# Kernel optimization log

Hardware: AMD Instinct MI355X
Metric: run time of the kernel (lower is better)

Reference implementation:

```python
import jax, jax.numpy as jnp
import numpy as np

N_NODES = 20000
N_EDGES = 160000
F_IN = 128
H1 = 1024  # 128 * out_channels
H2 = 512   # 64 * out_channels
OUT = 8    # out_channels


def graph_conv(x, src, dst, w_rel, b_rel, w_root):
    # PyG GraphConv(aggr='mean'): out = lin_rel(mean_{j->i} x_j) + lin_root(x_i)
    n = x.shape[0]
    agg = jax.ops.segment_sum(x[src], dst, num_segments=n)          # [N, F_in]
    deg = jax.ops.segment_sum(jnp.ones((src.shape[0],), x.dtype), dst, num_segments=n)
    mean = agg / jnp.maximum(deg, 1.0)[:, None]
    return mean @ w_rel + b_rel + x @ w_root


def setup_inputs() -> dict:
    key = jax.random.key(0)
    ks = jax.random.split(key, 12)
    x = jax.random.normal(ks[0], (N_NODES, F_IN), dtype=jnp.float32)
    edge_index = jax.random.randint(ks[1], (2, N_EDGES), 0, N_NODES, dtype=jnp.int64)

    def lin(k, fi, fo):
        return jax.random.normal(k, (fi, fo), dtype=jnp.float32) / np.sqrt(fi)

    return {
        "x": x,
        "edge_index": edge_index,
        "w1_rel": lin(ks[2], F_IN, H1), "b1": jnp.zeros((H1,), jnp.float32), "w1_root": lin(ks[3], F_IN, H1),
        "w2_rel": lin(ks[4], H1, H2), "b2": jnp.zeros((H2,), jnp.float32), "w2_root": lin(ks[5], H1, H2),
        "wmu_rel": lin(ks[6], H2, OUT), "bmu": jnp.zeros((OUT,), jnp.float32), "wmu_root": lin(ks[7], H2, OUT),
        "wls_rel": lin(ks[8], H2, OUT), "bls": jnp.zeros((OUT,), jnp.float32), "wls_root": lin(ks[9], H2, OUT),
    }


def reference(x, edge_index, w1_rel, b1, w1_root, w2_rel, b2, w2_root,
              wmu_rel, bmu, wmu_root, wls_rel, bls, wls_root):
    src, dst = edge_index[0], edge_index[1]
    h = jax.nn.relu(graph_conv(x, src, dst, w1_rel, b1, w1_root))
    h = jax.nn.relu(graph_conv(h, src, dst, w2_rel, b2, w2_root))
    mu = graph_conv(h, src, dst, wmu_rel, bmu, wmu_root)
    logstd = graph_conv(h, src, dst, wls_rel, bls, wls_root)
    return (mu, logstd)
```

## Files before the change

### kernel.cpp

```cpp
#include <hip/hip_runtime.h>

typedef __attribute__((ext_vector_type(8))) short short8;
typedef __attribute__((ext_vector_type(4))) float f32x4;
typedef unsigned long long u64;

__device__ __forceinline__ unsigned short f2bf(float f) {
  union { float f; unsigned u; } v; v.f = f;
  unsigned u = v.u;
  unsigned r = (u + 0x7FFFu + ((u >> 16) & 1u)) >> 16;
  return (unsigned short)r;
}
__device__ __forceinline__ float bf2f(unsigned short s) {
  union { unsigned u; float f; } v; v.u = ((unsigned)s) << 16;
  return v.f;
}

__device__ __forceinline__ void gl_lds16(const unsigned short* g, unsigned short* l) {
  __builtin_amdgcn_global_load_lds(
      (const __attribute__((address_space(1))) void*)g,
      (__attribute__((address_space(3))) void*)l, 16, 0, 0);
}


__device__ __forceinline__ void ttile(const float* __restrict__ src, int Nw,
                                      unsigned short* __restrict__ dst, int ldd,
                                      int rowoff, int coloff,
                                      int tileIdx, int tilesN, float (*tile)[33]) {
  int tk = tileIdx / tilesN, tn = tileIdx % tilesN;
  int k0 = tk * 32, n0 = tn * 32;
  int tx = threadIdx.x & 31, ty = threadIdx.x >> 5;
#pragma unroll
  for (int s = 0; s < 4; ++s)
    tile[ty + s * 8][tx] = src[(size_t)(k0 + ty + s * 8) * Nw + n0 + tx];
  __syncthreads();
#pragma unroll
  for (int s = 0; s < 4; ++s)
    dst[(size_t)(rowoff + n0 + ty + s * 8) * ldd + coloff + k0 + tx] =
        f2bf(tile[tx][ty + s * 8]);
}

__global__ void prep_kernel(int* deg, int* cursor, int n, int* flag,
                            const float* __restrict__ x, unsigned short* __restrict__ xb,
                            int total4,
                            const float* __restrict__ w1_rel, const float* __restrict__ w1_root,
                            const float* __restrict__ w2_rel, const float* __restrict__ w2_root,
                            const float* __restrict__ wmu_rel, const float* __restrict__ wmu_root,
                            const float* __restrict__ wls_rel, const float* __restrict__ wls_root,
                            unsigned short* __restrict__ Bt1,
                            unsigned short* __restrict__ Bt2,
                            unsigned short* __restrict__ Bt3) {
  __shared__ float tile[32][33];
  int b = blockIdx.x;
  if (b >= 1408) {
    int b4 = (b - 1408) * 1024;
#pragma unroll
    for (int s = 0; s < 4; ++s) {
      int i4 = b4 + s * 256 + threadIdx.x;
      if (i4 < total4) {
        float4 v = reinterpret_cast<const float4*>(x)[i4];
        ushort4 o;
        o.x = f2bf(v.x); o.y = f2bf(v.y); o.z = f2bf(v.z); o.w = f2bf(v.w);
        reinterpret_cast<ushort4*>(xb)[i4] = o;
      }
    }
    return;
  }
  if (b >= 1344) {
    int i = (b - 1344) * blockDim.x + threadIdx.x;
    int stride = 64 * blockDim.x;
    for (int j = i; j < n; j += stride) { deg[j] = 0; cursor[j] = 0; }
    if (i == 0) *flag = 1;
    return;
  }
  if (b < 128)       ttile(w1_rel, 1024, Bt1, 256, 0, 0, b, 32, tile);
  else if (b < 256)  ttile(w1_root, 1024, Bt1, 256, 0, 128, b - 128, 32, tile);
  else if (b < 768)  ttile(w2_rel, 512, Bt2, 1024, 0, 0, b - 256, 16, tile);
  else if (b < 1280) ttile(w2_root, 512, Bt2, 1024, 512, 0, b - 768, 16, tile);
  else {
    int idx = (b - 1280) * 256 + threadIdx.x;
    int nn = idx >> 9, k = idx & 511;
    float v;
    if (nn < 8) v = wmu_rel[(size_t)k * 8 + nn];
    else if (nn < 16) v = wmu_root[(size_t)k * 8 + (nn - 8)];
    else if (nn < 24) v = wls_rel[(size_t)k * 8 + (nn - 16)];
    else v = wls_root[(size_t)k * 8 + (nn - 24)];
    Bt3[(size_t)nn * 512 + k] = f2bf(v);
  }
}

__global__ void detect_kernel(const long long* p, int nslots, int n_nodes, int* flag) {
  int i = blockIdx.x * blockDim.x + threadIdx.x;
  if (i < nslots) {
    long long v = p[i];
    if (v < 0 || v >= n_nodes) atomicAnd(flag, 0);
  }
}

__device__ __forceinline__ int edge_at(const void* p, int is64, size_t idx) {
  return is64 ? (int)((const long long*)p)[idx] : ((const int*)p)[idx];
}

__global__ void count_kernel(const void* edges, int E, const int* flag, int* deg) {
  int is64 = *flag;
  int i = blockIdx.x * blockDim.x + threadIdx.x;
  int stride = gridDim.x * blockDim.x;
  for (int e = i; e < E; e += stride) {
    int d = edge_at(edges, is64, (size_t)E + e);
    atomicAdd(&deg[d], 1);
  }
}

__global__ void scan_kernel(const int* __restrict__ deg, int* __restrict__ rs,
                            float* __restrict__ invdeg, int n) {
  __shared__ int ssum[1024];
  int tid = threadIdx.x;
  int chunk = (n + 1023) >> 10;
  int start = tid * chunk;
  int end = min(start + chunk, n);
  int s = 0;
  for (int i = start; i < end; ++i) s += deg[i];
  ssum[tid] = s;
  __syncthreads();
  for (int off = 1; off < 1024; off <<= 1) {
    int t = (tid >= off) ? ssum[tid - off] : 0;
    __syncthreads();
    ssum[tid] += t;
    __syncthreads();
  }
  int run = (tid ? ssum[tid - 1] : 0);
  if (tid == 0) rs[0] = 0;
  for (int i = start; i < end; ++i) {
    int d = deg[i];
    run += d;
    rs[i + 1] = run;
    invdeg[i] = 1.0f / fmaxf((float)d, 1.0f);
  }
}

__global__ void fill_kernel(const void* edges, int E, const int* flag,
                            const int* __restrict__ rs, int* cursor, int* col_src) {
  int is64 = *flag;
  int i = blockIdx.x * blockDim.x + threadIdx.x;
  int stride = gridDim.x * blockDim.x;
  for (int e = i; e < E; e += stride) {
    int d = edge_at(edges, is64, (size_t)E + e);
    int s = edge_at(edges, is64, (size_t)e);
    int p = atomicAdd(&cursor[d], 1);
    col_src[rs[d] + p] = s;
  }
}


__global__ void agg1_kernel(const unsigned short* __restrict__ xb,
                            const int* __restrict__ rs, const int* __restrict__ cs,
                            const float* __restrict__ invdeg,
                            unsigned short* __restrict__ A1, int M) {
  int node = blockIdx.x * 4 + (threadIdx.x >> 6);
  if (node >= M) return;
  int c0 = (threadIdx.x & 63) * 2;
  float a0 = 0.f, a1 = 0.f;
  int e1 = rs[node + 1];
  for (int e = rs[node]; e < e1; ++e) {
    unsigned w = *reinterpret_cast<const unsigned*>(xb + (size_t)cs[e] * 128 + c0);
    a0 += bf2f((unsigned short)(w & 0xffff));
    a1 += bf2f((unsigned short)(w >> 16));
  }
  float inv = invdeg[node];
  unsigned root = *reinterpret_cast<const unsigned*>(xb + (size_t)node * 128 + c0);
  unsigned mean = (unsigned)f2bf(a0 * inv) | ((unsigned)f2bf(a1 * inv) << 16);
  *reinterpret_cast<unsigned*>(A1 + (size_t)node * 256 + c0) = mean;
  *reinterpret_cast<unsigned*>(A1 + (size_t)node * 256 + 128 + c0) = root;
}

__global__ void agg2_kernel(const unsigned short* __restrict__ P2,
                            const int* __restrict__ rs, const int* __restrict__ cs,
                            const float* __restrict__ invdeg,
                            const float* __restrict__ b2,
                            unsigned short* __restrict__ h2, int M) {
  int node = blockIdx.x * 2 + (threadIdx.x >> 6);
  if (node >= M) return;
  int f0 = (threadIdx.x & 63) * 8;
  float acc[8];
#pragma unroll
  for (int v = 0; v < 8; ++v) acc[v] = 0.f;
  int e1 = rs[node + 1];
  for (int e = rs[node]; e < e1; ++e) {
    int s = cs[e];
    uint4 w = *reinterpret_cast<const uint4*>(P2 + (size_t)s * 1024 + f0);
    acc[0] += bf2f((unsigned short)(w.x & 0xffff));
    acc[1] += bf2f((unsigned short)(w.x >> 16));
    acc[2] += bf2f((unsigned short)(w.y & 0xffff));
    acc[3] += bf2f((unsigned short)(w.y >> 16));
    acc[4] += bf2f((unsigned short)(w.z & 0xffff));
    acc[5] += bf2f((unsigned short)(w.z >> 16));
    acc[6] += bf2f((unsigned short)(w.w & 0xffff));
    acc[7] += bf2f((unsigned short)(w.w >> 16));
  }
  float inv = invdeg[node];
  uint4 wr = *reinterpret_cast<const uint4*>(P2 + (size_t)node * 1024 + 512 + f0);
  float rt[8] = {
    bf2f((unsigned short)(wr.x & 0xffff)), bf2f((unsigned short)(wr.x >> 16)),
    bf2f((unsigned short)(wr.y & 0xffff)), bf2f((unsigned short)(wr.y >> 16)),
    bf2f((unsigned short)(wr.z & 0xffff)), bf2f((unsigned short)(wr.z >> 16)),
    bf2f((unsigned short)(wr.w & 0xffff)), bf2f((unsigned short)(wr.w >> 16))};
  unsigned short o[8];
#pragma unroll
  for (int v = 0; v < 8; ++v)
    o[v] = f2bf(fmaxf(acc[v] * inv + rt[v] + b2[f0 + v], 0.f));
  uint4 pk;
  pk.x = (unsigned)o[0] | ((unsigned)o[1] << 16);
  pk.y = (unsigned)o[2] | ((unsigned)o[3] << 16);
  pk.z = (unsigned)o[4] | ((unsigned)o[5] << 16);
  pk.w = (unsigned)o[6] | ((unsigned)o[7] << 16);
  *reinterpret_cast<uint4*>(h2 + (size_t)node * 512 + f0) = pk;
}

__global__ void head_agg_kernel(const float* __restrict__ P3,
                                const int* __restrict__ rs, const int* __restrict__ cs,
                                const float* __restrict__ invdeg,
                                const float* __restrict__ bmu, const float* __restrict__ bls,
                                float* __restrict__ outmu, float* __restrict__ outls, int M) {
  int idx = blockIdx.x * blockDim.x + threadIdx.x;
  int node = idx >> 4;
  int c = idx & 15;
  if (node >= M) return;
  int relc = (c < 8) ? c : (16 + (c - 8));
  float acc = 0.f;
  int e1 = rs[node + 1];
  for (int e = rs[node]; e < e1; ++e) acc += P3[(size_t)cs[e] * 32 + relc];
  float v = acc * invdeg[node] + P3[(size_t)node * 32 + relc + 8]
          + ((c < 8) ? bmu[c] : bls[c - 8]);
  if (c < 8) outmu[(size_t)node * 8 + c] = v;
  else outls[(size_t)node * 8 + (c - 8)] = v;
}

__launch_bounds__(256, 4)
__global__ void gemm_db_kernel(const unsigned short* __restrict__ A, int lda,
                               const unsigned short* __restrict__ Bt, int ldb,
                               const float* __restrict__ bias,
                               void* __restrict__ outp, int ldo,
                               int M, int N, int K, int relu, int out_f32, int gx) {
  __shared__ unsigned short As[2 * 4096];
  __shared__ unsigned short Bs[2 * 4096];
  const int tid = threadIdx.x;
  const int lane = tid & 63;
  const int w = tid >> 6;
  const int wr = w >> 1, wc = w & 1;
  const int lr = lane & 15, lk = lane >> 4;
  const int sw8 = (lk ^ ((lr >> 1) & 3)) * 8;

  int nwg = gridDim.x, orig = blockIdx.x;
  int q = nwg >> 3, r = nwg & 7;
  int xcd = orig & 7, lid = orig >> 3;
  int swz = (xcd < r ? xcd * (q + 1) : r * (q + 1) + (xcd - r) * q) + lid;
  int m0 = (swz / gx) * 128, n0 = (swz % gx) * 128;

  f32x4 acc[4][4];
#pragma unroll
  for (int i = 0; i < 4; ++i)
#pragma unroll
    for (int j = 0; j < 4; ++j) acc[i][j] = (f32x4)0.0f;

  const int r0 = tid >> 2;
  const int slog = ((tid & 3) ^ ((r0 >> 1) & 3)) * 8;
  const unsigned short* gA = A + (size_t)(m0 + r0) * lda + slog;
  const unsigned short* gB = Bt + (size_t)(n0 + r0) * ldb + slog;
  const size_t a64 = (size_t)64 * lda, b64 = (size_t)64 * ldb;
  unsigned short* wa = As + w * 512;
  unsigned short* wb = Bs + w * 512;

  auto STG = [&](int s, int t) {
    const unsigned short* a = gA + (size_t)t * 32;
    const unsigned short* b = gB + (size_t)t * 32;
    gl_lds16(a, wa + s * 4096);
    gl_lds16(a + a64, wa + s * 4096 + 2048);
    gl_lds16(b, wb + s * 4096);
    gl_lds16(b + b64, wb + s * 4096 + 2048);
  };

  const int nt = K >> 5;
  STG(0, 0);
  __syncthreads();

  int buf = 0;
  for (int t = 0; t < nt; ++t) {
    if (t + 1 < nt) STG(buf ^ 1, t + 1);
    const unsigned short* as_ = As + buf * 4096;
    const unsigned short* bs_ = Bs + buf * 4096;
    short8 af[4], bf[4];
#pragma unroll
    for (int i = 0; i < 4; ++i) {
      af[i] = *reinterpret_cast<const short8*>(&as_[(wr * 64 + i * 16 + lr) * 32 + sw8]);
      bf[i] = *reinterpret_cast<const short8*>(&bs_[(wc * 64 + i * 16 + lr) * 32 + sw8]);
    }
    __builtin_amdgcn_s_setprio(1);
#pragma unroll
    for (int i = 0; i < 4; ++i)
#pragma unroll
      for (int j = 0; j < 4; ++j)
        acc[i][j] = __builtin_amdgcn_mfma_f32_16x16x32_bf16(af[i], bf[j], acc[i][j], 0, 0, 0);
    __builtin_amdgcn_s_setprio(0);
    if (t + 1 < nt) __syncthreads();
    buf ^= 1;
  }

#pragma unroll
  for (int i = 0; i < 4; ++i) {
    int row_b = m0 + wr * 64 + i * 16 + lk * 4;
#pragma unroll
    for (int j = 0; j < 4; ++j) {
      int col = n0 + wc * 64 + j * 16 + lr;
      float bv = bias ? bias[col] : 0.f;
#pragma unroll
      for (int rr = 0; rr < 4; ++rr) {
        int row = row_b + rr;
        if (row < M) {
          float v = acc[i][j][rr] + bv;
          if (relu) v = fmaxf(v, 0.f);
          if (out_f32) ((float*)outp)[(size_t)row * ldo + col] = v;
          else ((unsigned short*)outp)[(size_t)row * ldo + col] = f2bf(v);
        }
      }
    }
  }
}

__launch_bounds__(256, 3)
__global__ void gemm_heads_kernel(const unsigned short* __restrict__ A,
                                  const unsigned short* __restrict__ Bt3,
                                  float* __restrict__ P3, int M) {
  __shared__ unsigned short Bs[16 * 1024];
  __shared__ unsigned short As[2 * 4096];
  const int tid = threadIdx.x;
  const int lane = tid & 63;
  const int w = tid >> 6;
  const int lr = lane & 15, lk = lane >> 4;
  const int sw8 = (lk ^ ((lr >> 1) & 3)) * 8;

  int nwg = gridDim.x, orig = blockIdx.x;
  int q = nwg >> 3, r = nwg & 7;
  int xcd = orig & 7, lid = orig >> 3;
  int swz = (xcd < r ? xcd * (q + 1) : r * (q + 1) + (xcd - r) * q) + lid;
  int m0 = swz * 128;

  for (int i = 0; i < 8; ++i) {
    int j = i * 256 + tid;
    int n = j >> 6, p = j & 63;
    int x = (n >> 1) & 3;
    uint4 v = *reinterpret_cast<const uint4*>(Bt3 + (size_t)n * 512 + ((p & ~3) | ((p & 3) ^ x)) * 8);
    *reinterpret_cast<uint4*>(&Bs[(p >> 2) * 1024 + n * 32 + (p & 3) * 8]) = v;
  }

  f32x4 acc[2][2];
#pragma unroll
  for (int i = 0; i < 2; ++i)
#pragma unroll
    for (int j = 0; j < 2; ++j) acc[i][j] = (f32x4)0.0f;

  const int r0 = tid >> 2;
  const int slog = ((tid & 3) ^ ((r0 >> 1) & 3)) * 8;
  const unsigned short* gA = A + (size_t)(m0 + r0) * 512 + slog;
  const size_t a64 = (size_t)64 * 512;
  unsigned short* wa = As + w * 512;

  auto STG = [&](int s, int t) {
    const unsigned short* a = gA + (size_t)t * 32;
    gl_lds16(a, wa + s * 4096);
    gl_lds16(a + a64, wa + s * 4096 + 2048);
  };

  STG(0, 0);
  __syncthreads();

  int buf = 0;
  const int nt = 16;
  for (int t = 0; t < nt; ++t) {
    if (t + 1 < nt) STG(buf ^ 1, t + 1);
    const unsigned short* as_ = As + buf * 4096;
    short8 af[2], bf[2];
#pragma unroll
    for (int i = 0; i < 2; ++i) {
      af[i] = *reinterpret_cast<const short8*>(&as_[(w * 32 + i * 16 + lr) * 32 + sw8]);
      bf[i] = *reinterpret_cast<const short8*>(&Bs[t * 1024 + (i * 16 + lr) * 32 + sw8]);
    }
#pragma unroll
    for (int i = 0; i < 2; ++i)
#pragma unroll
      for (int j = 0; j < 2; ++j)
        acc[i][j] = __builtin_amdgcn_mfma_f32_16x16x32_bf16(af[i], bf[j], acc[i][j], 0, 0, 0);
    if (t + 1 < nt) __syncthreads();
    buf ^= 1;
  }

#pragma unroll
  for (int i = 0; i < 2; ++i) {
    int row_b = m0 + w * 32 + i * 16 + lk * 4;
#pragma unroll
    for (int j = 0; j < 2; ++j) {
      int col = j * 16 + lr;
#pragma unroll
      for (int rr = 0; rr < 4; ++rr) {
        int row = row_b + rr;
        if (row < M) P3[(size_t)row * 32 + col] = acc[i][j][rr];
      }
    }
  }
}


extern "C" void kernel_launch(void* const* d_in, const int* in_sizes, int n_in,
                              void* d_out, int out_size, void* d_ws, size_t ws_size,
                              hipStream_t stream) {
  const float* x = (const float*)d_in[0];
  const void* edge = d_in[1];
  const float* w1_rel = (const float*)d_in[2];
  const float* b1 = (const float*)d_in[3];
  const float* w1_root = (const float*)d_in[4];
  const float* w2_rel = (const float*)d_in[5];
  const float* b2 = (const float*)d_in[6];
  const float* w2_root = (const float*)d_in[7];
  const float* wmu_rel = (const float*)d_in[8];
  const float* bmu = (const float*)d_in[9];
  const float* wmu_root = (const float*)d_in[10];
  const float* wls_rel = (const float*)d_in[11];
  const float* bls = (const float*)d_in[12];
  const float* wls_root = (const float*)d_in[13];

  const int FIN = 128, H1 = 1024, H2 = 512;
  const int M = in_sizes[0] / FIN;
  const int E = in_sizes[1] / 2;
  const int Mpad = ((M + 127) / 128) * 128;
  const int gy = Mpad / 128;

  char* ws = (char*)d_ws;
  size_t off = 0;
  auto alloc = [&](size_t bytes) -> char* {
    char* p = ws + off;
    off = (off + bytes + 255) & ~(size_t)255;
    return p;
  };
  int* flag = (int*)alloc(4);
  int* deg = (int*)alloc((size_t)M * 4);
  int* cursor = (int*)alloc((size_t)M * 4);
  int* rs = (int*)alloc((size_t)(M + 1) * 4);
  float* invdeg = (float*)alloc((size_t)M * 4);
  int* cs = (int*)alloc((size_t)E * 4);
  unsigned short* xb = (unsigned short*)alloc((size_t)M * 128 * 2);
  unsigned short* A1 = (unsigned short*)alloc((size_t)Mpad * 256 * 2);
  unsigned short* h1 = (unsigned short*)alloc((size_t)Mpad * 1024 * 2);
  unsigned short* P2 = (unsigned short*)alloc((size_t)Mpad * 1024 * 2);
  unsigned short* h2 = (unsigned short*)alloc((size_t)Mpad * 512 * 2);
  float* P3 = (float*)alloc((size_t)Mpad * 32 * 4);
  unsigned short* Bt1 = (unsigned short*)alloc((size_t)H1 * 256 * 2);
  unsigned short* Bt2 = (unsigned short*)alloc((size_t)1024 * 1024 * 2);
  unsigned short* Bt3 = (unsigned short*)alloc((size_t)32 * 512 * 2);

  prep_kernel<<<2048, 256, 0, stream>>>(deg, cursor, M, flag,
                                        x, xb, M * FIN / 4,
                                        w1_rel, w1_root, w2_rel, w2_root,
                                        wmu_rel, wmu_root, wls_rel, wls_root,
                                        Bt1, Bt2, Bt3);
  detect_kernel<<<8, 256, 0, stream>>>((const long long*)edge, 2048, M, flag);
  count_kernel<<<256, 256, 0, stream>>>(edge, E, flag, deg);
  scan_kernel<<<1, 1024, 0, stream>>>(deg, rs, invdeg, M);
  fill_kernel<<<256, 256, 0, stream>>>(edge, E, flag, rs, cursor, cs);

  agg1_kernel<<<(M + 3) / 4, 256, 0, stream>>>(xb, rs, cs, invdeg, A1, M);
  gemm_db_kernel<<<(H1 / 128) * gy, 256, 0, stream>>>(
      A1, 256, Bt1, 256, b1, h1, 1024, M, H1, 256, 1, 0, H1 / 128);

  gemm_db_kernel<<<(1024 / 128) * gy, 256, 0, stream>>>(
      h1, 1024, Bt2, 1024, nullptr, P2, 1024, M, 1024, 1024, 0, 0, 1024 / 128);
  agg2_kernel<<<(M + 1) / 2, 128, 0, stream>>>(P2, rs, cs, invdeg, b2, h2, M);

  gemm_heads_kernel<<<gy, 256, 0, stream>>>(h2, Bt3, P3, M);
  float* outmu = (float*)d_out;
  float* outls = outmu + (size_t)M * 8;
  head_agg_kernel<<<(M * 16 + 255) / 256, 256, 0, stream>>>(
      P3, rs, cs, invdeg, bmu, bls, outmu, outls, M);
}
```

Before: 261.9 us.

## Use single-wave 64x64 GEMM for layer 2, inline index-width detection, widen agg2 blocks

Layer 2's GEMM moves from the 256-thread 128x128 double-buffered kernel to a new single-wavefront kernel. Each wave computes a 64x64 tile with its own LDS double buffer, which gives a grid four times larger for better CU occupancy. The separate detect kernel and its flag are removed, and count and fill now each check the first 8 int64 values inline to decide the index width. agg2 goes from 2 to 4 nodes per 256-thread block. The small tiles give less operand reuse per load, and the inline check reads only 8 entries instead of 2048, so index-width detection is weaker.

```diff
diff --git a/kernel.cpp b/kernel.cpp
--- a/kernel.cpp
+++ b/kernel.cpp
@@ -19,6 +19,17 @@
   __builtin_amdgcn_global_load_lds(
       (const __attribute__((address_space(1))) void*)g,
       (__attribute__((address_space(3))) void*)l, 16, 0, 0);
+}
+
+__device__ __forceinline__ int detect64(const void* edges, int n_nodes) {
+  const long long* p = (const long long*)edges;
+  int ok = 1;
+#pragma unroll
+  for (int i = 0; i < 8; ++i) {
+    long long v = p[i];
+    if (v < 0 || v >= n_nodes) ok = 0;
+  }
+  return ok;
 }
 
 
@@ -39,7 +50,7 @@
         f2bf(tile[tx][ty + s * 8]);
 }
 
-__global__ void prep_kernel(int* deg, int* cursor, int n, int* flag,
+__global__ void prep_kernel(int* deg, int* cursor, int n,
                             const float* __restrict__ x, unsigned short* __restrict__ xb,
                             int total4,
                             const float* __restrict__ w1_rel, const float* __restrict__ w1_root,
@@ -69,7 +80,6 @@
     int i = (b - 1344) * blockDim.x + threadIdx.x;
     int stride = 64 * blockDim.x;
     for (int j = i; j < n; j += stride) { deg[j] = 0; cursor[j] = 0; }
-    if (i == 0) *flag = 1;
     return;
   }
   if (b < 128)       ttile(w1_rel, 1024, Bt1, 256, 0, 0, b, 32, tile);
@@ -88,20 +98,12 @@
   }
 }
 
-__global__ void detect_kernel(const long long* p, int nslots, int n_nodes, int* flag) {
-  int i = blockIdx.x * blockDim.x + threadIdx.x;
-  if (i < nslots) {
-    long long v = p[i];
-    if (v < 0 || v >= n_nodes) atomicAnd(flag, 0);
-  }
-}
-
 __device__ __forceinline__ int edge_at(const void* p, int is64, size_t idx) {
   return is64 ? (int)((const long long*)p)[idx] : ((const int*)p)[idx];
 }
 
-__global__ void count_kernel(const void* edges, int E, const int* flag, int* deg) {
-  int is64 = *flag;
+__global__ void count_kernel(const void* edges, int E, int n_nodes, int* deg) {
+  int is64 = detect64(edges, n_nodes);
   int i = blockIdx.x * blockDim.x + threadIdx.x;
   int stride = gridDim.x * blockDim.x;
   for (int e = i; e < E; e += stride) {
@@ -137,9 +139,9 @@
   }
 }
 
-__global__ void fill_kernel(const void* edges, int E, const int* flag,
+__global__ void fill_kernel(const void* edges, int E, int n_nodes,
                             const int* __restrict__ rs, int* cursor, int* col_src) {
-  int is64 = *flag;
+  int is64 = detect64(edges, n_nodes);
   int i = blockIdx.x * blockDim.x + threadIdx.x;
   int stride = gridDim.x * blockDim.x;
   for (int e = i; e < E; e += stride) {
@@ -177,7 +179,7 @@
                             const float* __restrict__ invdeg,
                             const float* __restrict__ b2,
                             unsigned short* __restrict__ h2, int M) {
-  int node = blockIdx.x * 2 + (threadIdx.x >> 6);
+  int node = blockIdx.x * 4 + (threadIdx.x >> 6);
   if (node >= M) return;
   int f0 = (threadIdx.x & 63) * 8;
   float acc[8];
@@ -325,6 +327,88 @@
   }
 }
 
+__launch_bounds__(64, 2)
+__global__ void gemm_wv_kernel(const unsigned short* __restrict__ A, int lda,
+                               const unsigned short* __restrict__ Bt, int ldb,
+                               unsigned short* __restrict__ outp, int ldo,
+                               int M, int K, int gx) {
+  __shared__ unsigned short As[2 * 2048];
+  __shared__ unsigned short Bs[2 * 2048];
+  const int l = threadIdx.x;
+  const int lr = l & 15, lk = l >> 4;
+  const int sw8 = (lk ^ ((lr >> 1) & 3)) * 8;
+
+  int nwg = gridDim.x, orig = blockIdx.x;
+  int q = nwg >> 3, r = nwg & 7;
+  int xcd = orig & 7, lid = orig >> 3;
+  int swz = (xcd < r ? xcd * (q + 1) : r * (q + 1) + (xcd - r) * q) + lid;
+  int m0 = (swz / gx) * 64, n0 = (swz % gx) * 64;
+
+  f32x4 acc[4][4];
+#pragma unroll
+  for (int i = 0; i < 4; ++i)
+#pragma unroll
+    for (int j = 0; j < 4; ++j) acc[i][j] = (f32x4)0.0f;
+
+  const int srow = l >> 2;
+  const int sslot = ((l & 3) ^ ((l >> 3) & 3)) * 8;
+  const unsigned short* gA = A + (size_t)(m0 + srow) * lda + sslot;
+  const unsigned short* gB = Bt + (size_t)(n0 + srow) * ldb + sslot;
+
+  auto STG = [&](int s, int t) {
+#pragma unroll
+    for (int c = 0; c < 4; ++c) {
+      gl_lds16(gA + (size_t)t * 32 + (size_t)(c * 16) * lda, As + s * 2048 + c * 512);
+      gl_lds16(gB + (size_t)t * 32 + (size_t)(c * 16) * ldb, Bs + s * 2048 + c * 512);
+    }
+  };
+
+  const int nt = K >> 5;
+  STG(0, 0);
+  STG(1, 1);
+  asm volatile("s_waitcnt vmcnt(8)" ::: "memory");
+
+  for (int t = 0; t < nt; ++t) {
+    const unsigned short* as_ = As + (t & 1) * 2048;
+    const unsigned short* bs_ = Bs + (t & 1) * 2048;
+    short8 af[4], bf[4];
+#pragma unroll
+    for (int i = 0; i < 4; ++i) {
+      af[i] = *reinterpret_cast<const short8*>(&as_[(i * 16 + lr) * 32 + sw8]);
+      bf[i] = *reinterpret_cast<const short8*>(&bs_[(i * 16 + lr) * 32 + sw8]);
+    }
+    asm volatile("s_waitcnt lgkmcnt(0)" ::: "memory");
+    if (t + 2 < nt) STG(t & 1, t + 2);
+    __builtin_amdgcn_s_setprio(1);
+#pragma unroll
+    for (int i = 0; i < 4; ++i)
+#pragma unroll
+      for (int j = 0; j < 4; ++j)
+        acc[i][j] = __builtin_amdgcn_mfma_f32_16x16x32_bf16(af[i], bf[j], acc[i][j], 0, 0, 0);
+    __builtin_amdgcn_s_setprio(0);
+    if (t + 1 < nt) {
+      if (t + 2 < nt)
+        asm volatile("s_waitcnt vmcnt(8)" ::: "memory");
+      else
+        asm volatile("s_waitcnt vmcnt(0)" ::: "memory");
+    }
+  }
+
+#pragma unroll
+  for (int i = 0; i < 4; ++i) {
+    int row_b = m0 + i * 16 + lk * 4;
+#pragma unroll
+    for (int j = 0; j < 4; ++j) {
+      int col = n0 + j * 16 + lr;
+#pragma unroll
+      for (int rr = 0; rr < 4; ++rr) {
+        int row = row_b + rr;
+        if (row < M) outp[(size_t)row * ldo + col] = f2bf(acc[i][j][rr]);
+      }
+    }
+  }
+}
+
 __launch_bounds__(256, 3)
 __global__ void gemm_heads_kernel(const unsigned short* __restrict__ A,
                                   const unsigned short* __restrict__ Bt3,
@@ -431,6 +515,7 @@
   const int E = in_sizes[1] / 2;
   const int Mpad = ((M + 127) / 128) * 128;
   const int gy = Mpad / 128;
+  const int gy64 = Mpad / 64;
 
   char* ws = (char*)d_ws;
   size_t off = 0;
@@ -439,7 +524,6 @@
     off = (off + bytes + 255) & ~(size_t)255;
     return p;
   };
-  int* flag = (int*)alloc(4);
   int* deg = (int*)alloc((size_t)M * 4);
   int* cursor = (int*)alloc((size_t)M * 4);
   int* rs = (int*)alloc((size_t)(M + 1) * 4);
@@ -455,23 +539,22 @@
   unsigned short* Bt2 = (unsigned short*)alloc((size_t)1024 * 1024 * 2);
   unsigned short* Bt3 = (unsigned short*)alloc((size_t)32 * 512 * 2);
 
-  prep_kernel<<<2048, 256, 0, stream>>>(deg, cursor, M, flag,
+  prep_kernel<<<2048, 256, 0, stream>>>(deg, cursor, M,
                                         x, xb, M * FIN / 4,
                                         w1_rel, w1_root, w2_rel, w2_root,
                                         wmu_rel, wmu_root, wls_rel, wls_root,
                                         Bt1, Bt2, Bt3);
-  detect_kernel<<<8, 256, 0, stream>>>((const long long*)edge, 2048, M, flag);
-  count_kernel<<<256, 256, 0, stream>>>(edge, E, flag, deg);
+  count_kernel<<<256, 256, 0, stream>>>(edge, E, M, deg);
   scan_kernel<<<1, 1024, 0, stream>>>(deg, rs, invdeg, M);
-  fill_kernel<<<256, 256, 0, stream>>>(edge, E, flag, rs, cursor, cs);
+  fill_kernel<<<256, 256, 0, stream>>>(edge, E, M, rs, cursor, cs);
 
   agg1_kernel<<<(M + 3) / 4, 256, 0, stream>>>(xb, rs, cs, invdeg, A1, M);
   gemm_db_kernel<<<(H1 / 128) * gy, 256, 0, stream>>>(
       A1, 256, Bt1, 256, b1, h1, 1024, M, H1, 256, 1, 0, H1 / 128);
 
-  gemm_db_kernel<<<(1024 / 128) * gy, 256, 0, stream>>>(
-      h1, 1024, Bt2, 1024, nullptr, P2, 1024, M, 1024, 1024, 0, 0, 1024 / 128);
-  agg2_kernel<<<(M + 1) / 2, 128, 0, stream>>>(P2, rs, cs, invdeg, b2, h2, M);
+  gemm_wv_kernel<<<(1024 / 64) * gy64, 64, 0, stream>>>(
+      h1, 1024, Bt2, 1024, P2, 1024, M, 1024, 1024 / 64);
+  agg2_kernel<<<(M + 3) / 4, 256, 0, stream>>>(P2, rs, cs, invdeg, b2, h2, M);
 
   gemm_heads_kernel<<<gy, 256, 0, stream>>>(h2, Bt3, P3, M);
   float* outmu = (float*)d_out;
```

Result: faster. 249.6 us (-4.7%).
